# Kernel optimization log

Hardware: AMD Instinct MI355X
Metric: run time of the kernel (lower is better)

Reference implementation:

```python
import jax, jax.numpy as jnp
import numpy as np

N_NODES = 100000
N_EDGES = 3200000


def _spmm(edge_row, edge_col, edge_val, h):
    # out[i] = sum_{e: row[e]==i} val[e] * h[col[e]]
    msgs = edge_val[:, None] * h[edge_col]  # [E, F]
    return jax.ops.segment_sum(msgs, edge_row, num_segments=N_NODES)


def _gc_layer(x, W, b, edge_row, edge_col, edge_val):
    # GraphConvolution: support = x @ W; out = spmm(adj, support) + b
    support = x @ W
    return _spmm(edge_row, edge_col, edge_val, support) + b


def setup_inputs() -> dict:
    key = jax.random.key(0)
    ks = jax.random.split(key, 8)
    F_IN, HID, C = 512, 256, 40
    x = jax.random.normal(ks[0], (N_NODES, F_IN), dtype=jnp.float32)
    W1 = jax.random.normal(ks[1], (F_IN, HID), dtype=jnp.float32) * (1.0 / np.sqrt(F_IN))
    b1 = jnp.zeros((HID,), dtype=jnp.float32)
    W2 = jax.random.normal(ks[2], (HID, C), dtype=jnp.float32) * (1.0 / np.sqrt(HID))
    b2 = jnp.zeros((C,), dtype=jnp.float32)
    edge_row = jax.random.randint(ks[3], (N_EDGES,), 0, N_NODES, dtype=jnp.int32)
    edge_col = jax.random.randint(ks[4], (N_EDGES,), 0, N_NODES, dtype=jnp.int32)
    edge_val = jax.random.uniform(ks[5], (N_EDGES,), dtype=jnp.float32) * 0.05
    return {"x": x, "W1": W1, "b1": b1, "W2": W2, "b2": b2,
            "edge_row": edge_row, "edge_col": edge_col, "edge_val": edge_val}


def reference(x, W1, b1, W2, b2, edge_row, edge_col, edge_val):
    h = jax.nn.relu(_gc_layer(x, W1, b1, edge_row, edge_col, edge_val))
    # dropout: inference mode (training=False) -> identity
    logits = _gc_layer(h, W2, b2, edge_row, edge_col, edge_val)
    return (jax.nn.log_softmax(logits, axis=1), jax.nn.softmax(logits, axis=1))
```

## Files before the change

kernel.cpp:

```cpp
#include <hip/hip_runtime.h>
#include <hip/hip_bf16.h>

#define N_NODES 100000
#define N_EDGES 3200000
#define F_IN    512
#define HID     256
#define C_OUT   40

#define RPB     512
#define BSHIFT  9
#define NBUCK   196
#define CAP     20480
#define GSTR    16

typedef unsigned short u16;
typedef unsigned char  u8;
typedef __attribute__((ext_vector_type(4))) unsigned short u16x4;
typedef __attribute__((ext_vector_type(8))) short bf16x8;
typedef __attribute__((ext_vector_type(4))) float f32x4;
typedef __attribute__((ext_vector_type(2))) float f32x2;

__device__ __forceinline__ float bf2f(u16 u) {
    unsigned int x = ((unsigned int)u) << 16;
    return __uint_as_float(x);
}
__device__ __forceinline__ u16 f2bf(float f) {
    unsigned int x = __float_as_uint(f);
    return (u16)((x + 0x7fffu + ((x >> 16) & 1u)) >> 16);
}
__device__ __forceinline__ unsigned int pk2(float lo, float hi) {
    return (unsigned int)f2bf(lo) | ((unsigned int)f2bf(hi) << 16);
}
__device__ __forceinline__ u8 f2fp8(float f) {
    return (u8)(__builtin_amdgcn_cvt_pk_fp8_f32(f, f, 0u, false) & 0xFF);
}


__global__ __launch_bounds__(1024) void k_p1(const int* __restrict__ row,
                                             const int* __restrict__ col,
                                             const float* __restrict__ val,
                                             int* __restrict__ gfill,
                                             int2* __restrict__ bpack) {
    __shared__ int hist[NBUCK];
    __shared__ int base[NBUCK];
    int t = threadIdx.x;
    for (int j = t; j < NBUCK; j += 1024) hist[j] = 0;
    __syncthreads();
    int e0 = blockIdx.x * 4096;
    int bin[4], key[4], lr[4];
    float vl[4];
#pragma unroll
    for (int u = 0; u < 4; u++) {
        int i = e0 + u * 1024 + t;
        if (i < N_EDGES) {
            int r = row[i];
            bin[u] = r >> BSHIFT;
            key[u] = (col[i] << BSHIFT) | (r & (RPB - 1));
            vl[u] = val[i];
            lr[u] = atomicAdd(&hist[bin[u]], 1);
        } else {
            bin[u] = -1;
        }
    }
    __syncthreads();
    for (int j = t; j < NBUCK; j += 1024)
        base[j] = atomicAdd(&gfill[j * GSTR], hist[j]);
    __syncthreads();
#pragma unroll
    for (int u = 0; u < 4; u++) {
        if (bin[u] >= 0) {
            int p = base[bin[u]] + lr[u];
            if (p < CAP)
                bpack[(size_t)bin[u] * CAP + p] = make_int2(key[u], __float_as_int(vl[u]));
        }
    }
}

__global__ void k_bscan(const int* __restrict__ gfill,
                        int* __restrict__ bucket_base,
                        int* __restrict__ row_off) {
    if (threadIdx.x == 0 && blockIdx.x == 0) {
        int run = 0;
        for (int b = 0; b < NBUCK; b++) {
            bucket_base[b] = run;
            run += gfill[b * GSTR];
        }
        row_off[N_NODES] = run;
    }
}

__global__ __launch_bounds__(1024) void k_p2(const int2* __restrict__ bpack,
                                             const int* __restrict__ gfill,
                                             const int* __restrict__ bucket_base,
                                             int2* __restrict__ cpack,
                                             int* __restrict__ row_off) {
    __shared__ int cnt[RPB];
    __shared__ int sc[RPB];
    __shared__ int rbase[RPB];
    int b = blockIdx.x, t = threadIdx.x;
    int n = gfill[b * GSTR];
    if (n > CAP) n = CAP;
    int gbase = bucket_base[b];
    if (t < RPB) cnt[t] = 0;
    __syncthreads();
    int key[20], lr[20];
    float v[20];
#pragma unroll
    for (int u = 0; u < 20; u++) {
        int i = u * 1024 + t;
        if (i < n) {
            int2 p = bpack[(size_t)b * CAP + i];
            key[u] = p.x;
            v[u] = __int_as_float(p.y);
            lr[u] = atomicAdd(&cnt[key[u] & (RPB - 1)], 1);
        } else {
            key[u] = -1;
        }
    }
    __syncthreads();
    if (t < RPB) sc[t] = cnt[t];
    __syncthreads();
    for (int off = 1; off < RPB; off <<= 1) {
        int x = 0;
        if (t < RPB && t >= off) x = sc[t - off];
        __syncthreads();
        if (t < RPB) sc[t] += x;
        __syncthreads();
    }
    if (t < RPB) rbase[t] = (t == 0) ? 0 : sc[t - 1];
    __syncthreads();
    int g0 = b * RPB;
    if (t < RPB && (g0 + t) < N_NODES) row_off[g0 + t] = gbase + rbase[t];
#pragma unroll
    for (int u = 0; u < 20; u++) {
        if (key[u] >= 0) {
            int pos = gbase + rbase[key[u] & (RPB - 1)] + lr[u];
            cpack[pos] = make_int2(key[u] >> BSHIFT, __float_as_int(v[u]));
        }
    }
}


__global__ __launch_bounds__(256) void k_cvtW1(const float* __restrict__ W1,
                                               u16* __restrict__ W1t) {
    int i = blockIdx.x * 256 + threadIdx.x;
    int k = i >> 8, n = i & 255;
    W1t[(size_t)n * F_IN + k] = f2bf(W1[i]);
}

__global__ __launch_bounds__(256) void k_cvtW2(const float* __restrict__ W2,
                                               u16* __restrict__ W2t) {
    int i = blockIdx.x * 256 + threadIdx.x;
    int n = i >> 8, k = i & 255;
    W2t[i] = (n < C_OUT) ? f2bf(W2[k * C_OUT + n]) : (u16)0;
}


#define ASTR 40
#define BSTR 40

__global__ __launch_bounds__(512) void k_gemm1(const float* __restrict__ A,
                                               const u16* __restrict__ Bt,
                                               u8* __restrict__ Cf8, int M) {
    __shared__ u16 As[2][128 * ASTR];
    __shared__ u16 Bs[2][256 * BSTR];
    int tid = threadIdx.x;
    int bm = blockIdx.x * 128;
    int lane = tid & 63, wid = tid >> 6;
    int wm = wid >> 2, wn = wid & 3;

    int s_ar = tid >> 2;
    int s_ak = (tid & 3) * 8;
    int s_bn = tid >> 1;
    int s_bk = (tid & 1) * 16;

    bool arow_ok = (bm + s_ar) < M;
    const float* aptr = A + (size_t)(bm + s_ar) * F_IN + s_ak;
    const u16*   bptr = Bt + (size_t)s_bn * F_IN + s_bk;

    f32x4 acc[4][4];
#pragma unroll
    for (int i = 0; i < 4; i++)
#pragma unroll
        for (int j = 0; j < 4; j++) acc[i][j] = (f32x4){0.f, 0.f, 0.f, 0.f};

    float4 ra0, ra1;
    int4 rb0, rb1;

    auto LOAD = [&](int kt) {
        const float* ap = aptr + kt * 32;
        if (arow_ok) {
            ra0 = *(const float4*)ap;
            ra1 = *(const float4*)(ap + 4);
        } else {
            ra0 = make_float4(0.f, 0.f, 0.f, 0.f);
            ra1 = ra0;
        }
        const u16* bp = bptr + kt * 32;
        rb0 = *(const int4*)bp;
        rb1 = *(const int4*)(bp + 8);
    };
    auto WRITE = [&](int buf) {
        int4 w;
        w.x = pk2(ra0.x, ra0.y);
        w.y = pk2(ra0.z, ra0.w);
        w.z = pk2(ra1.x, ra1.y);
        w.w = pk2(ra1.z, ra1.w);
        *(int4*)&As[buf][s_ar * ASTR + s_ak] = w;
        *(int4*)&Bs[buf][s_bn * BSTR + s_bk] = rb0;
        *(int4*)&Bs[buf][s_bn * BSTR + s_bk + 8] = rb1;
    };

    int kg = lane >> 4;
    int r16 = lane & 15;

    auto COMPUTE = [&](int buf) {
        bf16x8 a[4], b[4];
#pragma unroll
        for (int mt = 0; mt < 4; mt++)
            a[mt] = *(const bf16x8*)&As[buf][(wm * 64 + mt * 16 + r16) * ASTR + kg * 8];
#pragma unroll
        for (int nt = 0; nt < 4; nt++)
            b[nt] = *(const bf16x8*)&Bs[buf][(wn * 64 + nt * 16 + r16) * BSTR + kg * 8];
#pragma unroll
        for (int mt = 0; mt < 4; mt++)
#pragma unroll
            for (int nt = 0; nt < 4; nt++)
                acc[mt][nt] = __builtin_amdgcn_mfma_f32_16x16x32_bf16(
                    a[mt], b[nt], acc[mt][nt], 0, 0, 0);
    };

    LOAD(0);
    WRITE(0);
    __syncthreads();
#pragma unroll 1
    for (int kt = 0; kt < F_IN / 32; kt++) {
        int cur = kt & 1;
        if (kt < F_IN / 32 - 1) LOAD(kt + 1);
        COMPUTE(cur);
        if (kt < F_IN / 32 - 1) WRITE(cur ^ 1);
        __syncthreads();
    }

#pragma unroll
    for (int mt = 0; mt < 4; mt++) {
        int r0 = bm + wm * 64 + mt * 16 + (lane >> 4) * 4;
#pragma unroll
        for (int nt = 0; nt < 4; nt++) {
            int c = wn * 64 + nt * 16 + (lane & 15);
#pragma unroll
            for (int j = 0; j < 4; j++) {
                int r = r0 + j;
                if (r < M) Cf8[(size_t)r * HID + c] = f2fp8(acc[mt][nt][j]);
            }
        }
    }
}


__global__ __launch_bounds__(256) void k_spmm1(const u8* __restrict__ Sf8,
                                               const int2* __restrict__ cpack,
                                               const int* __restrict__ row_off,
                                               const float* __restrict__ b1,
                                               u16* __restrict__ Hb) {
    int lane = threadIdx.x & 63;
    int row = blockIdx.x * 4 + (threadIdx.x >> 6);
    int beg = __builtin_amdgcn_readfirstlane(row_off[row]);
    int end = __builtin_amdgcn_readfirstlane(row_off[row + 1]);
    int f4 = lane * 4;
    const u8* base = Sf8 + f4;
    float acc[4] = {};
    int e = beg;
    for (; e + 16 <= end; e += 16) {
        int2 q[16];
#pragma unroll
        for (int t = 0; t < 16; t++) q[t] = cpack[e + t];
#pragma unroll
        for (int t = 0; t < 16; t++) {
            float vv = __int_as_float(q[t].y);
            unsigned int w = *(const unsigned int*)(base + (size_t)q[t].x * HID);
            f32x2 lo = __builtin_amdgcn_cvt_pk_f32_fp8(w, false);
            f32x2 hi = __builtin_amdgcn_cvt_pk_f32_fp8(w, true);
            acc[0] += vv * lo.x;
            acc[1] += vv * lo.y;
            acc[2] += vv * hi.x;
            acc[3] += vv * hi.y;
        }
    }
    for (; e + 8 <= end; e += 8) {
        int2 q[8];
#pragma unroll
        for (int t = 0; t < 8; t++) q[t] = cpack[e + t];
#pragma unroll
        for (int t = 0; t < 8; t++) {
            float vv = __int_as_float(q[t].y);
            unsigned int w = *(const unsigned int*)(base + (size_t)q[t].x * HID);
            f32x2 lo = __builtin_amdgcn_cvt_pk_f32_fp8(w, false);
            f32x2 hi = __builtin_amdgcn_cvt_pk_f32_fp8(w, true);
            acc[0] += vv * lo.x;
            acc[1] += vv * lo.y;
            acc[2] += vv * hi.x;
            acc[3] += vv * hi.y;
        }
    }
    for (; e < end; e++) {
        int2 q = cpack[e];
        float vv = __int_as_float(q.y);
        unsigned int w = *(const unsigned int*)(base + (size_t)q.x * HID);
        f32x2 lo = __builtin_amdgcn_cvt_pk_f32_fp8(w, false);
        f32x2 hi = __builtin_amdgcn_cvt_pk_f32_fp8(w, true);
        acc[0] += vv * lo.x;
        acc[1] += vv * lo.y;
        acc[2] += vv * hi.x;
        acc[3] += vv * hi.y;
    }
    float4 b = *(const float4*)&b1[f4];
    u16x4 o;
    o.x = f2bf(fmaxf(acc[0] + b.x, 0.f));
    o.y = f2bf(fmaxf(acc[1] + b.y, 0.f));
    o.z = f2bf(fmaxf(acc[2] + b.z, 0.f));
    o.w = f2bf(fmaxf(acc[3] + b.w, 0.f));
    *(u16x4*)&Hb[(size_t)row * HID + f4] = o;
}


#define G2STR 264

__global__ __launch_bounds__(256) void k_gemm2(const u16* __restrict__ Hb,
                                               const u16* __restrict__ W2t,
                                               u8* __restrict__ S2f8) {
    __shared__ u16 As[64 * G2STR];
    int tid = threadIdx.x;
    int base = blockIdx.x * 64;
    {
        int r = tid >> 2, c0 = (tid & 3) * 64;
        const u16* src = Hb + (size_t)(base + r) * HID + c0;
        bool ok = (base + r) < N_NODES;
#pragma unroll
        for (int q = 0; q < 8; q++) {
            int4 d = ok ? *(const int4*)(src + q * 8) : make_int4(0, 0, 0, 0);
            *(int4*)&As[r * G2STR + c0 + q * 8] = d;
        }
    }
    __syncthreads();
    int lane = tid & 63, wv = tid >> 6;
    int r16 = lane & 15, kg = lane >> 4;
    f32x4 acc[4];
#pragma unroll
    for (int nt = 0; nt < 4; nt++) acc[nt] = (f32x4){0.f, 0.f, 0.f, 0.f};
#pragma unroll
    for (int ks = 0; ks < 8; ks++) {
        bf16x8 a = *(const bf16x8*)&As[(wv * 16 + r16) * G2STR + ks * 32 + kg * 8];
#pragma unroll
        for (int nt = 0; nt < 4; nt++) {
            bf16x8 b = *(const bf16x8*)&W2t[(size_t)(nt * 16 + r16) * 256 + ks * 32 + kg * 8];
            acc[nt] = __builtin_amdgcn_mfma_f32_16x16x32_bf16(a, b, acc[nt], 0, 0, 0);
        }
    }
    int orow = base + wv * 16 + (lane >> 4) * 4;
#pragma unroll
    for (int nt = 0; nt < 4; nt++) {
        int c = nt * 16 + r16;
        if (c < C_OUT) {
#pragma unroll
            for (int j = 0; j < 4; j++) {
                int r = orow + j;
                if (r < N_NODES) S2f8[(size_t)r * C_OUT + c] = f2fp8(acc[nt][j]);
            }
        }
    }
}


__global__ __launch_bounds__(256) void k_spmm2(const u8* __restrict__ S2f8,
                                               const int2* __restrict__ cpack,
                                               const int* __restrict__ row_off,
                                               const float* __restrict__ b2,
                                               float* __restrict__ out_ls,
                                               float* __restrict__ out_sm) {
    __shared__ float red[4][64][4];
    int tid = threadIdx.x;
    int lane = tid & 63, wv = tid >> 6;
    int row = blockIdx.x * 4 + wv;
    int beg = __builtin_amdgcn_readfirstlane(row_off[row]);
    int end = __builtin_amdgcn_readfirstlane(row_off[row + 1]);
    int g = lane / 10;
    int cb = (lane % 10) * 4;
    bool act = lane < 60;
    float acc[4] = {};
    for (int e0 = beg; e0 < end; e0 += 6) {
        int ei = e0 + g;
        bool ok = act && (ei < end);
        int2 q = cpack[ok ? ei : beg];
        float vv = ok ? __int_as_float(q.y) : 0.f;
        unsigned int w = *(const unsigned int*)(S2f8 + (size_t)q.x * C_OUT + cb);
        f32x2 lo = __builtin_amdgcn_cvt_pk_f32_fp8(w, false);
        f32x2 hi = __builtin_amdgcn_cvt_pk_f32_fp8(w, true);
        acc[0] += vv * lo.x;
        acc[1] += vv * lo.y;
        acc[2] += vv * hi.x;
        acc[3] += vv * hi.y;
    }
#pragma unroll
    for (int j = 0; j < 4; j++) red[wv][lane][j] = acc[j];
    __builtin_amdgcn_s_waitcnt(0);
    float v;
    if (lane < C_OUT) {
        int sl = lane >> 2, j = lane & 3;
        float s = 0.f;
#pragma unroll
        for (int gg = 0; gg < 6; gg++) s += red[wv][gg * 10 + sl][j];
        v = s + b2[lane];
    } else {
        v = -1e30f;
    }
    float mx = v;
    for (int s = 32; s; s >>= 1) mx = fmaxf(mx, __shfl_xor(mx, s));
    float e2 = (lane < C_OUT) ? __expf(v - mx) : 0.f;
    float sum = e2;
    for (int s = 32; s; s >>= 1) sum += __shfl_xor(sum, s);
    float ls = v - mx - __logf(sum);
    float sm = e2 / sum;
    if (lane < C_OUT) {
        out_ls[(size_t)row * C_OUT + lane] = ls;
        out_sm[(size_t)row * C_OUT + lane] = sm;
    }
}


extern "C" void kernel_launch(void* const* d_in, const int* in_sizes, int n_in,
                              void* d_out, int out_size, void* d_ws, size_t ws_size,
                              hipStream_t stream) {
    const float* x    = (const float*)d_in[0];
    const float* W1   = (const float*)d_in[1];
    const float* b1   = (const float*)d_in[2];
    const float* W2   = (const float*)d_in[3];
    const float* b2   = (const float*)d_in[4];
    const int*   erow = (const int*)d_in[5];
    const int*   ecol = (const int*)d_in[6];
    const float* eval = (const float*)d_in[7];
    float* out = (float*)d_out;

    char* w = (char*)d_ws;
    auto alloc = [&](size_t bytes) {
        char* p = w;
        w += (bytes + 255) & ~(size_t)255;
        return p;
    };
    u8*    support = (u8*)   alloc((size_t)N_NODES * HID);
    u16*   hbuf    = (u16*)  alloc((size_t)N_NODES * HID * sizeof(u16));
    int2*  cpack   = (int2*) alloc((size_t)N_EDGES * sizeof(int2));
    int2*  bpack   = (int2*) alloc((size_t)NBUCK * CAP * sizeof(int2));
    int*   row_off = (int*)  alloc((size_t)(N_NODES + 1) * sizeof(int));
    int*   gfill   = (int*)  alloc((size_t)NBUCK * GSTR * sizeof(int));
    int*   bucket_base = (int*) alloc((size_t)NBUCK * sizeof(int));
    u8*    S2f8    = (u8*)   alloc((size_t)N_NODES * C_OUT);
    u16*   W2t     = (u16*)  alloc((size_t)64 * 256 * sizeof(u16));
    u16*   W1t     = (u16*)  alloc((size_t)F_IN * HID * sizeof(u16));

    hipMemsetAsync(gfill, 0, (size_t)NBUCK * GSTR * sizeof(int), stream);

    int NB1 = (N_EDGES + 4095) / 4096;
    k_p1<<<NB1, 1024, 0, stream>>>(erow, ecol, eval, gfill, bpack);
    k_bscan<<<1, 64, 0, stream>>>(gfill, bucket_base, row_off);
    k_p2<<<NBUCK, 1024, 0, stream>>>(bpack, gfill, bucket_base, cpack, row_off);

    k_cvtW1<<<(F_IN * HID) / 256, 256, 0, stream>>>(W1, W1t);
    k_cvtW2<<<(64 * 256) / 256, 256, 0, stream>>>(W2, W2t);
    k_gemm1<<<(N_NODES + 127) / 128, 512, 0, stream>>>(x, W1t, support, N_NODES);
    k_spmm1<<<N_NODES / 4, 256, 0, stream>>>(support, cpack, row_off, b1, hbuf);
    k_gemm2<<<(N_NODES + 63) / 64, 256, 0, stream>>>(hbuf, W2t, S2f8);
    k_spmm2<<<N_NODES / 4, 256, 0, stream>>>(S2f8, cpack, row_off, b2,
                                             out, out + (size_t)N_NODES * C_OUT);
}
```

Before: 382.4 us.

## Fuse prep kernels, fold bucket scan into p2, store hidden as fp8, pack epilogues

The weight conversions and the gfill zeroing are merged into a single prep kernel, and the single-thread bucket scan moves inside k_p2 as a per-block shared-memory scan. Together these remove several small launches and a memset. The hidden activation is now stored as fp8 instead of bf16, halving its write and read traffic, and k_gemm2 widens it back to bf16 when loading. The GEMM operands are swapped so each lane holds four consecutive columns and can write one packed 32-bit fp8 word instead of four byte stores. The spmm1 unroll of 16 is dropped. Storing the hidden layer in fp8 lowers precision, which could affect accuracy.

```diff
diff --git a/kernel.cpp b/kernel.cpp
--- a/kernel.cpp
+++ b/kernel.cpp
@@ -15,24 +15,37 @@
 
 typedef unsigned short u16;
 typedef unsigned char  u8;
-typedef __attribute__((ext_vector_type(4))) unsigned short u16x4;
+typedef unsigned int   u32;
 typedef __attribute__((ext_vector_type(8))) short bf16x8;
 typedef __attribute__((ext_vector_type(4))) float f32x4;
 typedef __attribute__((ext_vector_type(2))) float f32x2;
 
-__device__ __forceinline__ float bf2f(u16 u) {
-    unsigned int x = ((unsigned int)u) << 16;
-    return __uint_as_float(x);
-}
 __device__ __forceinline__ u16 f2bf(float f) {
-    unsigned int x = __float_as_uint(f);
+    u32 x = __float_as_uint(f);
     return (u16)((x + 0x7fffu + ((x >> 16) & 1u)) >> 16);
 }
-__device__ __forceinline__ unsigned int pk2(float lo, float hi) {
-    return (unsigned int)f2bf(lo) | ((unsigned int)f2bf(hi) << 16);
-}
-__device__ __forceinline__ u8 f2fp8(float f) {
-    return (u8)(__builtin_amdgcn_cvt_pk_fp8_f32(f, f, 0u, false) & 0xFF);
+__device__ __forceinline__ u32 pk2(float lo, float hi) {
+    return (u32)f2bf(lo) | ((u32)f2bf(hi) << 16);
+}
+
+
+__global__ __launch_bounds__(256) void k_prep(const float* __restrict__ W1,
+                                              const float* __restrict__ W2,
+                                              u16* __restrict__ W1t,
+                                              u16* __restrict__ W2t,
+                                              int* __restrict__ gfill) {
+    int b = blockIdx.x, t = threadIdx.x;
+    if (b < 512) {
+        int i = b * 256 + t;
+        int k = i >> 8, n = i & 255;
+        W1t[(size_t)n * F_IN + k] = f2bf(W1[i]);
+    } else if (b < 576) {
+        int i = (b - 512) * 256 + t;
+        int n = i >> 8, k = i & 255;
+        W2t[i] = (n < C_OUT) ? f2bf(W2[k * C_OUT + n]) : (u16)0;
+    } else {
+        for (int j = t; j < NBUCK * GSTR; j += 256) gfill[j] = 0;
+    }
 }
 
 
@@ -76,31 +89,28 @@
     }
 }
 
-__global__ void k_bscan(const int* __restrict__ gfill,
-                        int* __restrict__ bucket_base,
-                        int* __restrict__ row_off) {
-    if (threadIdx.x == 0 && blockIdx.x == 0) {
-        int run = 0;
-        for (int b = 0; b < NBUCK; b++) {
-            bucket_base[b] = run;
-            run += gfill[b * GSTR];
-        }
-        row_off[N_NODES] = run;
-    }
-}
-
 __global__ __launch_bounds__(1024) void k_p2(const int2* __restrict__ bpack,
                                              const int* __restrict__ gfill,
-                                             const int* __restrict__ bucket_base,
                                              int2* __restrict__ cpack,
                                              int* __restrict__ row_off) {
+    __shared__ int bb[256];
     __shared__ int cnt[RPB];
     __shared__ int sc[RPB];
     __shared__ int rbase[RPB];
     int b = blockIdx.x, t = threadIdx.x;
+    if (t < 256) bb[t] = (t < NBUCK) ? gfill[t * GSTR] : 0;
+    __syncthreads();
+    for (int off = 1; off < 256; off <<= 1) {
+        int x = 0;
+        if (t < 256 && t >= off) x = bb[t - off];
+        __syncthreads();
+        if (t < 256) bb[t] += x;
+        __syncthreads();
+    }
+    int gbase = (b == 0) ? 0 : bb[b - 1];
+    if (b == NBUCK - 1 && t == 0) row_off[N_NODES] = bb[NBUCK - 1];
     int n = gfill[b * GSTR];
     if (n > CAP) n = CAP;
-    int gbase = bucket_base[b];
     if (t < RPB) cnt[t] = 0;
     __syncthreads();
     int key[20], lr[20];
@@ -138,21 +148,6 @@
             cpack[pos] = make_int2(key[u] >> BSHIFT, __float_as_int(v[u]));
         }
     }
-}
-
-
-__global__ __launch_bounds__(256) void k_cvtW1(const float* __restrict__ W1,
-                                               u16* __restrict__ W1t) {
-    int i = blockIdx.x * 256 + threadIdx.x;
-    int k = i >> 8, n = i & 255;
-    W1t[(size_t)n * F_IN + k] = f2bf(W1[i]);
-}
-
-__global__ __launch_bounds__(256) void k_cvtW2(const float* __restrict__ W2,
-                                               u16* __restrict__ W2t) {
-    int i = blockIdx.x * 256 + threadIdx.x;
-    int n = i >> 8, k = i & 255;
-    W2t[i] = (n < C_OUT) ? f2bf(W2[k * C_OUT + n]) : (u16)0;
 }
 
 
@@ -227,7 +222,7 @@
 #pragma unroll
             for (int nt = 0; nt < 4; nt++)
                 acc[mt][nt] = __builtin_amdgcn_mfma_f32_16x16x32_bf16(
-                    a[mt], b[nt], acc[mt][nt], 0, 0, 0);
+                    b[nt], a[mt], acc[mt][nt], 0, 0, 0);
     };
 
     LOAD(0);
@@ -244,14 +239,14 @@
 
 #pragma unroll
     for (int mt = 0; mt < 4; mt++) {
-        int r0 = bm + wm * 64 + mt * 16 + (lane >> 4) * 4;
-#pragma unroll
-        for (int nt = 0; nt < 4; nt++) {
-            int c = wn * 64 + nt * 16 + (lane & 15);
-#pragma unroll
-            for (int j = 0; j < 4; j++) {
-                int r = r0 + j;
-                if (r < M) Cf8[(size_t)r * HID + c] = f2fp8(acc[mt][nt][j]);
+        int xr = bm + wm * 64 + mt * 16 + (lane & 15);
+        if (xr < M) {
+#pragma unroll
+            for (int nt = 0; nt < 4; nt++) {
+                int wc0 = wn * 64 + nt * 16 + (lane >> 4) * 4;
+                u32 d = __builtin_amdgcn_cvt_pk_fp8_f32(acc[mt][nt][0], acc[mt][nt][1], 0u, false);
+                d = __builtin_amdgcn_cvt_pk_fp8_f32(acc[mt][nt][2], acc[mt][nt][3], d, true);
+                *(u32*)&Cf8[(size_t)xr * HID + wc0] = d;
             }
         }
     }
@@ -262,7 +257,7 @@
                                                const int2* __restrict__ cpack,
                                                const int* __restrict__ row_off,
                                                const float* __restrict__ b1,
-                                               u16* __restrict__ Hb) {
+                                               u8* __restrict__ Hb8) {
     int lane = threadIdx.x & 63;
     int row = blockIdx.x * 4 + (threadIdx.x >> 6);
     int beg = __builtin_amdgcn_readfirstlane(row_off[row]);
@@ -271,14 +266,14 @@
     const u8* base = Sf8 + f4;
     float acc[4] = {};
     int e = beg;
-    for (; e + 16 <= end; e += 16) {
-        int2 q[16];
-#pragma unroll
-        for (int t = 0; t < 16; t++) q[t] = cpack[e + t];
-#pragma unroll
-        for (int t = 0; t < 16; t++) {
+    for (; e + 8 <= end; e += 8) {
+        int2 q[8];
+#pragma unroll
+        for (int t = 0; t < 8; t++) q[t] = cpack[e + t];
+#pragma unroll
+        for (int t = 0; t < 8; t++) {
             float vv = __int_as_float(q[t].y);
-            unsigned int w = *(const unsigned int*)(base + (size_t)q[t].x * HID);
+            u32 w = *(const u32*)(base + (size_t)q[t].x * HID);
             f32x2 lo = __builtin_amdgcn_cvt_pk_f32_fp8(w, false);
             f32x2 hi = __builtin_amdgcn_cvt_pk_f32_fp8(w, true);
             acc[0] += vv * lo.x;
@@ -287,26 +282,10 @@
             acc[3] += vv * hi.y;
         }
     }
-    for (; e + 8 <= end; e += 8) {
-        int2 q[8];
-#pragma unroll
-        for (int t = 0; t < 8; t++) q[t] = cpack[e + t];
-#pragma unroll
-        for (int t = 0; t < 8; t++) {
-            float vv = __int_as_float(q[t].y);
-            unsigned int w = *(const unsigned int*)(base + (size_t)q[t].x * HID);
-            f32x2 lo = __builtin_amdgcn_cvt_pk_f32_fp8(w, false);
-            f32x2 hi = __builtin_amdgcn_cvt_pk_f32_fp8(w, true);
-            acc[0] += vv * lo.x;
-            acc[1] += vv * lo.y;
-            acc[2] += vv * hi.x;
-            acc[3] += vv * hi.y;
-        }
-    }
     for (; e < end; e++) {
         int2 q = cpack[e];
         float vv = __int_as_float(q.y);
-        unsigned int w = *(const unsigned int*)(base + (size_t)q.x * HID);
+        u32 w = *(const u32*)(base + (size_t)q.x * HID);
         f32x2 lo = __builtin_amdgcn_cvt_pk_f32_fp8(w, false);
         f32x2 hi = __builtin_amdgcn_cvt_pk_f32_fp8(w, true);
         acc[0] += vv * lo.x;
@@ -315,18 +294,19 @@
         acc[3] += vv * hi.y;
     }
     float4 b = *(const float4*)&b1[f4];
-    u16x4 o;
-    o.x = f2bf(fmaxf(acc[0] + b.x, 0.f));
-    o.y = f2bf(fmaxf(acc[1] + b.y, 0.f));
-    o.z = f2bf(fmaxf(acc[2] + b.z, 0.f));
-    o.w = f2bf(fmaxf(acc[3] + b.w, 0.f));
-    *(u16x4*)&Hb[(size_t)row * HID + f4] = o;
+    float h0 = fmaxf(acc[0] + b.x, 0.f);
+    float h1 = fmaxf(acc[1] + b.y, 0.f);
+    float h2 = fmaxf(acc[2] + b.z, 0.f);
+    float h3 = fmaxf(acc[3] + b.w, 0.f);
+    u32 d = __builtin_amdgcn_cvt_pk_fp8_f32(h0, h1, 0u, false);
+    d = __builtin_amdgcn_cvt_pk_fp8_f32(h2, h3, d, true);
+    *(u32*)&Hb8[(size_t)row * HID + f4] = d;
 }
 
 
 #define G2STR 264
 
-__global__ __launch_bounds__(256) void k_gemm2(const u16* __restrict__ Hb,
+__global__ __launch_bounds__(256) void k_gemm2(const u8* __restrict__ Hb8,
                                                const u16* __restrict__ W2t,
                                                u8* __restrict__ S2f8) {
     __shared__ u16 As[64 * G2STR];
@@ -334,12 +314,22 @@
     int base = blockIdx.x * 64;
     {
         int r = tid >> 2, c0 = (tid & 3) * 64;
-        const u16* src = Hb + (size_t)(base + r) * HID + c0;
+        const u8* src = Hb8 + (size_t)(base + r) * HID + c0;
         bool ok = (base + r) < N_NODES;
 #pragma unroll
-        for (int q = 0; q < 8; q++) {
-            int4 d = ok ? *(const int4*)(src + q * 8) : make_int4(0, 0, 0, 0);
-            *(int4*)&As[r * G2STR + c0 + q * 8] = d;
+        for (int q = 0; q < 4; q++) {
+            uint4 dv = ok ? *(const uint4*)(src + q * 16) : make_uint4(0, 0, 0, 0);
+            u32 wbuf[8];
+            u32 dd[4] = {dv.x, dv.y, dv.z, dv.w};
+#pragma unroll
+            for (int j = 0; j < 4; j++) {
+                f32x2 lo = __builtin_amdgcn_cvt_pk_f32_fp8(dd[j], false);
+                f32x2 hi = __builtin_amdgcn_cvt_pk_f32_fp8(dd[j], true);
+                wbuf[2 * j]     = pk2(lo.x, lo.y);
+                wbuf[2 * j + 1] = pk2(hi.x, hi.y);
+            }
+            *(int4*)&As[r * G2STR + c0 + q * 16]     = *(int4*)&wbuf[0];
+            *(int4*)&As[r * G2STR + c0 + q * 16 + 8] = *(int4*)&wbuf[4];
         }
     }
     __syncthreads();
@@ -354,18 +344,18 @@
 #pragma unroll
         for (int nt = 0; nt < 4; nt++) {
             bf16x8 b = *(const bf16x8*)&W2t[(size_t)(nt * 16 + r16) * 256 + ks * 32 + kg * 8];
-            acc[nt] = __builtin_amdgcn_mfma_f32_16x16x32_bf16(a, b, acc[nt], 0, 0, 0);
-        }
-    }
-    int orow = base + wv * 16 + (lane >> 4) * 4;
-#pragma unroll
-    for (int nt = 0; nt < 4; nt++) {
-        int c = nt * 16 + r16;
-        if (c < C_OUT) {
-#pragma unroll
-            for (int j = 0; j < 4; j++) {
-                int r = orow + j;
-                if (r < N_NODES) S2f8[(size_t)r * C_OUT + c] = f2fp8(acc[nt][j]);
+            acc[nt] = __builtin_amdgcn_mfma_f32_16x16x32_bf16(b, a, acc[nt], 0, 0, 0);
+        }
+    }
+    int hr = base + wv * 16 + (lane & 15);
+    if (hr < N_NODES) {
+#pragma unroll
+        for (int nt = 0; nt < 3; nt++) {
+            int cls0 = nt * 16 + (lane >> 4) * 4;
+            if (cls0 < C_OUT) {
+                u32 d = __builtin_amdgcn_cvt_pk_fp8_f32(acc[nt][0], acc[nt][1], 0u, false);
+                d = __builtin_amdgcn_cvt_pk_fp8_f32(acc[nt][2], acc[nt][3], d, true);
+                *(u32*)&S2f8[(size_t)hr * C_OUT + cls0] = d;
             }
         }
     }
@@ -393,7 +383,7 @@
         bool ok = act && (ei < end);
         int2 q = cpack[ok ? ei : beg];
         float vv = ok ? __int_as_float(q.y) : 0.f;
-        unsigned int w = *(const unsigned int*)(S2f8 + (size_t)q.x * C_OUT + cb);
+        u32 w = *(const u32*)(S2f8 + (size_t)q.x * C_OUT + cb);
         f32x2 lo = __builtin_amdgcn_cvt_pk_f32_fp8(w, false);
         f32x2 hi = __builtin_amdgcn_cvt_pk_f32_fp8(w, true);
         acc[0] += vv * lo.x;
@@ -448,28 +438,24 @@
         return p;
     };
     u8*    support = (u8*)   alloc((size_t)N_NODES * HID);
-    u16*   hbuf    = (u16*)  alloc((size_t)N_NODES * HID * sizeof(u16));
+    u8*    hbuf8   = (u8*)   alloc((size_t)N_NODES * HID);
     int2*  cpack   = (int2*) alloc((size_t)N_EDGES * sizeof(int2));
     int2*  bpack   = (int2*) alloc((size_t)NBUCK * CAP * sizeof(int2));
     int*   row_off = (int*)  alloc((size_t)(N_NODES + 1) * sizeof(int));
     int*   gfill   = (int*)  alloc((size_t)NBUCK * GSTR * sizeof(int));
-    int*   bucket_base = (int*) alloc((size_t)NBUCK * sizeof(int));
     u8*    S2f8    = (u8*)   alloc((size_t)N_NODES * C_OUT);
     u16*   W2t     = (u16*)  alloc((size_t)64 * 256 * sizeof(u16));
     u16*   W1t     = (u16*)  alloc((size_t)F_IN * HID * sizeof(u16));
 
-    hipMemsetAsync(gfill, 0, (size_t)NBUCK * GSTR * sizeof(int), stream);
+    k_prep<<<577, 256, 0, stream>>>(W1, W2, W1t, W2t, gfill);
 
     int NB1 = (N_EDGES + 4095) / 4096;
     k_p1<<<NB1, 1024, 0, stream>>>(erow, ecol, eval, gfill, bpack);
-    k_bscan<<<1, 64, 0, stream>>>(gfill, bucket_base, row_off);
-    k_p2<<<NBUCK, 1024, 0, stream>>>(bpack, gfill, bucket_base, cpack, row_off);
-
-    k_cvtW1<<<(F_IN * HID) / 256, 256, 0, stream>>>(W1, W1t);
-    k_cvtW2<<<(64 * 256) / 256, 256, 0, stream>>>(W2, W2t);
+    k_p2<<<NBUCK, 1024, 0, stream>>>(bpack, gfill, cpack, row_off);
+
     k_gemm1<<<(N_NODES + 127) / 128, 512, 0, stream>>>(x, W1t, support, N_NODES);
-    k_spmm1<<<N_NODES / 4, 256, 0, stream>>>(support, cpack, row_off, b1, hbuf);
-    k_gemm2<<<(N_NODES + 63) / 64, 256, 0, stream>>>(hbuf, W2t, S2f8);
+    k_spmm1<<<N_NODES / 4, 256, 0, stream>>>(support, cpack, row_off, b1, hbuf8);
+    k_gemm2<<<(N_NODES + 63) / 64, 256, 0, stream>>>(hbuf8, W2t, S2f8);
     k_spmm2<<<N_NODES / 4, 256, 0, stream>>>(S2f8, cpack, row_off, b2,
                                              out, out + (size_t)N_NODES * C_OUT);
 }
```

Result: no change. 375.9 us (-1.7%).
